# Kernel optimization log

Measured on AMD Instinct MI355X. Metric: run time of the kernel, lower is better.

Reference implementation:

```python
import jax, jax.numpy as jnp
import numpy as np

B, N, SEM, STR = 64, 512, 256, 256  # batch, tokens, sem_dim_size, str_dim_size (hidden=512)


def setup_inputs() -> dict:
    key = jax.random.key(0)
    ks = jax.random.split(key, 8)
    s = 0.02  # small init so exp(f_ij)/exp(f_i) stay well-conditioned
    return {
        "input": jax.random.normal(ks[0], (B, N, SEM + STR), jnp.float32),
        "Wp": (jax.random.normal(ks[1], (STR, STR), jnp.float32) * s),
        "bp": jnp.zeros((STR,), jnp.float32),
        "Wbil": (jax.random.normal(ks[2], (STR, STR), jnp.float32) * s),
        "bbil": jnp.zeros((), jnp.float32),
        "Wfi": (jax.random.normal(ks[3], (1, STR), jnp.float32) * s),
        "bfi": jnp.zeros((1,), jnp.float32),
        "exparam": jax.random.normal(ks[4], (1, 1, SEM), jnp.float32),
        "Wfz": (jax.random.normal(ks[5], (SEM, 2 * SEM), jnp.float32) * s),
        "bfz": jnp.zeros((SEM,), jnp.float32),
    }


def reference(input, Wp, bp, Wbil, bbil, Wfi, bfi, exparam, Wfz, bfz):
    b, n, _ = input.shape
    sem_v = input[:, :, :SEM]          # [B,N,SEM]
    str_v = input[:, :, SEM:]          # [B,N,STR]

    # NOTE: source uses tp_linear for BOTH tp and tc, and expands both with
    # unsqueeze(2), so f_ij[b,i,j] = bilinear(tp[b,i], tp[b,i]) is constant in j.
    tp = str_v @ Wp.T + bp             # [B,N,STR]
    s = jnp.einsum('bid,de,bie->bi', tp, Wbil, tp) + bbil   # [B,N]
    f_ij = jnp.broadcast_to(s[:, :, None], (b, n, n))        # [B,N,N]

    f_i = jnp.exp(str_v @ Wfi.T + bfi)[..., 0]               # [B,N]

    off = 1.0 - jnp.eye(n, dtype=input.dtype)
    A = jnp.exp(f_ij) * off                                  # zero diagonal
    deg = jnp.sum(A, axis=2)                                 # [B,N]
    L = -A + deg[:, :, None] * jnp.eye(n, dtype=input.dtype) # Laplacian
    L = L.at[:, 0, :].set(f_i)                               # root-augmented L_bar

    LLinv = jnp.linalg.inv(L)                                # [B,N,N]
    d0 = f_i * LLinv[:, :, 0]                                # root marginals [B,N]
    dg = jnp.diagonal(LLinv, axis1=-2, axis2=-1)             # [B,N]

    # tmp1 and tmp2 in the source both reduce to A[b,i,j] * diag[b,j]
    tmp = A * dg[:, None, :]
    mask1 = jnp.concatenate([jnp.zeros((n, 1)), jnp.ones((n, n - 1))], 1).astype(input.dtype)
    mask2 = jnp.concatenate([jnp.zeros((1, n)), jnp.ones((n - 1, n))], 0).astype(input.dtype)
    dx = (mask1 - mask2) * tmp                               # [B,N,N]

    d = jnp.concatenate([d0[:, None, :], dx], axis=1)        # [B,N+1,N]
    df = jnp.swapaxes(d, 1, 2)                               # [B,N,N+1]
    ssr = jnp.concatenate([jnp.broadcast_to(exparam, (b, 1, SEM)), sem_v], 1)  # [B,N+1,SEM]
    pinp = jnp.einsum('bnm,bmd->bnd', df, ssr)               # [B,N,SEM]
    # cinp = dx @ sem_v is computed in the source but never used -> omitted

    finp = jnp.concatenate([sem_v, pinp], axis=-1)           # [B,N,2*SEM]
    return jax.nn.relu(finp @ Wfz.T + bfz)                   # [B,N,SEM]
```

## Files before the change

kernel.cpp:

```cpp
#include <hip/hip_runtime.h>
#include <math.h>

#define B_    64
#define N_    512
#define SEM_  256
#define STR_  256
#define DIM_  512
#define ROWS_ (B_*N_)

#define OFF_T      0
#define OFF_QT16   65536
#define OFF_W116   98304
#define OFF_W2T    131072
#define OFF_V1     196608
#define OFF_C1     196864
#define OFF_H      197120
#define OFF_C0     197376
#define OFF_EV     197440
#define OFF_FV     230208
#define OFF_SUMP   262976
#define OFF_V2B    394048
#define OFF_ROW0   410432

typedef __bf16 bf16x8 __attribute__((ext_vector_type(8)));
typedef float  f32x4  __attribute__((ext_vector_type(4)));

__device__ __forceinline__ ushort f2b(float x) {
    return __builtin_bit_cast(ushort, (__bf16)x);
}
__device__ __forceinline__ float bflo(unsigned u) {
    return __builtin_bit_cast(float, u << 16);
}
__device__ __forceinline__ float bfhi(unsigned u) {
    return __builtin_bit_cast(float, u & 0xffff0000u);
}

__global__ __launch_bounds__(256) void k0a(
    const float* __restrict__ Wp, const float* __restrict__ bp,
    const float* __restrict__ Wbil, const float* __restrict__ Wfz,
    const float* __restrict__ exparam,
    float* __restrict__ T, ushort* __restrict__ W116, float* __restrict__ W2t,
    float* __restrict__ v1, float* __restrict__ h, float* __restrict__ c0)
{
    int t = threadIdx.x, a = blockIdx.x;
    float acc = 0.f;
    const float* wb = Wbil + a*256;
    for (int c = 0; c < 256; ++c) acc += wb[c] * Wp[c*256 + t];
    T[a*256 + t] = acc;
    W116[a*256 + t] = f2b(Wfz[a*512 + t]);
    W2t[t*256 + a] = Wfz[a*512 + 256 + t];
    if (a == 0) {
        float s = 0.f;
        const float* w2 = Wfz + t*512 + 256;
        for (int dd = 0; dd < 256; ++dd) s += w2[dd] * exparam[dd];
        v1[t] = s;
    }
    if (a == 1) {
        float g = 0.f, g2 = 0.f;
        for (int c = 0; c < 256; ++c) {
            g  += Wbil[t*256 + c] * bp[c];
            g2 += Wbil[c*256 + t] * bp[c];
        }
        h[t] = g + g2;
        __shared__ float red[256];
        red[t] = bp[t] * g;
        __syncthreads();
        for (int s2 = 128; s2 > 0; s2 >>= 1) {
            if (t < s2) red[t] += red[t + s2];
            __syncthreads();
        }
        if (t == 0) c0[0] = red[0];
    }
}

__global__ __launch_bounds__(256) void k0b(
    const float* __restrict__ Wp, const float* __restrict__ T,
    const float* __restrict__ h,
    ushort* __restrict__ Qt16, float* __restrict__ c1)
{
    int t = threadIdx.x, d = blockIdx.x;
    float acc = 0.f;
    for (int a2 = 0; a2 < 256; ++a2) acc += Wp[a2*256 + d] * T[a2*256 + t];
    Qt16[t*256 + d] = f2b(acc);
    __shared__ float red[256];
    red[t] = Wp[t*256 + d] * h[t];
    __syncthreads();
    for (int s2 = 128; s2 > 0; s2 >>= 1) {
        if (t < s2) red[t] += red[t + s2];
        __syncthreads();
    }
    if (t == 0) c1[d] = red[0];
}

__global__ __launch_bounds__(256, 3) void k_rowstats(
    const float* __restrict__ input, const ushort* __restrict__ Qt16,
    const float* __restrict__ c1, const float* __restrict__ c0,
    const float* __restrict__ Wfi, const float* __restrict__ bbil,
    const float* __restrict__ bfi, const float* __restrict__ W2t,
    float* __restrict__ Ev, float* __restrict__ fv, float* __restrict__ v2b)
{
    __shared__ __align__(16) char smem[52288];
    ushort* Ash   = (ushort*)smem;
    ushort* Ush   = (ushort*)(smem + 32768);
    float*  sdiag = (float*)(smem + 49152);
    float*  fdiag = (float*)(smem + 50176);
    float*  s0sh  = (float*)(smem + 51200);
    float*  shE0  = (float*)(smem + 52224);

    int t = threadIdx.x;
    int lane = t & 63, w = t >> 6;
    int g = lane >> 4, li = lane & 15;
    long rowbase = (long)blockIdx.x * 64;
    int b = (int)(rowbase >> 9);
    int i0 = (int)(rowbase & 511);
    const float* Ab = input + rowbase*DIM_ + SEM_;

#pragma unroll
    for (int q = 0; q < 16; ++q) {
        int v = t + 256*q;
        int r = v >> 6, c4 = v & 63;
        float4 a4 = *(const float4*)(Ab + (long)r*DIM_ + c4*4);
        ushort4 b4 = make_ushort4(f2b(a4.x), f2b(a4.y), f2b(a4.z), f2b(a4.w));
        *(ushort4*)&Ash[r*256 + ((c4*4) ^ ((r & 7) << 3))] = b4;
    }
    __syncthreads();

    f32x4 acc[4][4];
#pragma unroll
    for (int m = 0; m < 4; ++m)
#pragma unroll
        for (int n = 0; n < 4; ++n) acc[m][n] = (f32x4){0.f, 0.f, 0.f, 0.f};

    int xs = (li & 7) << 3;
#pragma unroll 2
    for (int k0 = 0; k0 < 256; k0 += 32) {
        bf16x8 af[4], bfr[4];
#pragma unroll
        for (int n = 0; n < 4; ++n)
            bfr[n] = *(const bf16x8*)&Qt16[(w*64 + n*16 + li)*256 + k0 + g*8];
#pragma unroll
        for (int m = 0; m < 4; ++m)
            af[m] = *(const bf16x8*)&Ash[(m*16 + li)*256 + ((k0 + g*8) ^ xs)];
#pragma unroll
        for (int m = 0; m < 4; ++m)
#pragma unroll
            for (int n = 0; n < 4; ++n)
                acc[m][n] = __builtin_amdgcn_mfma_f32_16x16x32_bf16(af[m], bfr[n], acc[m][n], 0, 0, 0);
    }

    float c1v[4];
#pragma unroll
    for (int n = 0; n < 4; ++n) c1v[n] = c1[w*64 + n*16 + li];

    f32x4 dacc[4], facc[4];
#pragma unroll
    for (int m = 0; m < 4; ++m) { dacc[m] = (f32x4){0.f,0.f,0.f,0.f}; facc[m] = (f32x4){0.f,0.f,0.f,0.f}; }

#pragma unroll
    for (int h = 0; h < 2; ++h) {
        if ((w >> 1) == h) {
            int cl0 = (w & 1)*64;
#pragma unroll
            for (int m = 0; m < 4; ++m)
#pragma unroll
                for (int n = 0; n < 4; ++n)
#pragma unroll
                    for (int reg = 0; reg < 4; ++reg) {
                        int row = m*16 + g*4 + reg;
                        int cl = cl0 + n*16 + li;
                        Ush[row*128 + (cl ^ ((row & 7) << 3))] = f2b(acc[m][n][reg] + c1v[n]);
                    }
        }
        __syncthreads();
        int kb = w*32 + g*8;
        int kg = h*128 + kb;
        float4 wf0 = *(const float4*)(Wfi + kg);
        float4 wf1 = *(const float4*)(Wfi + kg + 4);
        bf16x8 afw = (bf16x8){(__bf16)wf0.x, (__bf16)wf0.y, (__bf16)wf0.z, (__bf16)wf0.w,
                              (__bf16)wf1.x, (__bf16)wf1.y, (__bf16)wf1.z, (__bf16)wf1.w};
#pragma unroll
        for (int m = 0; m < 4; ++m) {
            bf16x8 afu = *(const bf16x8*)&Ush[(m*16 + li)*128 + (kb ^ xs)];
            bf16x8 bfs = *(const bf16x8*)&Ash[(m*16 + li)*256 + (kg ^ xs)];
            dacc[m] = __builtin_amdgcn_mfma_f32_16x16x32_bf16(afu, bfs, dacc[m], 0, 0, 0);
            facc[m] = __builtin_amdgcn_mfma_f32_16x16x32_bf16(afw, bfs, facc[m], 0, 0, 0);
        }
        __syncthreads();
    }

    if (g == (li >> 2)) {
        int dr = li & 3;
#pragma unroll
        for (int m = 0; m < 4; ++m) {
            float dv = dr == 0 ? dacc[m][0] : dr == 1 ? dacc[m][1] : dr == 2 ? dacc[m][2] : dacc[m][3];
            sdiag[(m*16 + li)*4 + w] = dv;
        }
    }
    if (g == 0) {
#pragma unroll
        for (int m = 0; m < 4; ++m) fdiag[(m*16 + li)*4 + w] = facc[m][0];
    }
    __syncthreads();
    if (t < 64) {
        float ss = sdiag[t*4] + sdiag[t*4+1] + sdiag[t*4+2] + sdiag[t*4+3];
        float ff = fdiag[t*4] + fdiag[t*4+1] + fdiag[t*4+2] + fdiag[t*4+3];
        float ev = expf(ss + c0[0] + bbil[0]);
        Ev[rowbase + t] = ev;
        fv[rowbase + t] = expf(ff + bfi[0]);
        if (t == 0) shE0[0] = ev;
    }

    if (i0 == 0) {
        if (t < 64)
            *(float4*)&s0sh[t*4] = *(const float4*)(input + (long)b*512*DIM_ + t*4);
        __syncthreads();
        float a2 = 0.f;
        for (int d = 0; d < 256; ++d) a2 += W2t[d*256 + t] * s0sh[d];
        v2b[b*256 + t] = shE0[0] * a2;
    }
}

__global__ __launch_bounds__(256, 3) void k_final(
    const float* __restrict__ input, const ushort* __restrict__ W116,
    const float* __restrict__ v1, const float* __restrict__ v2b,
    const float* __restrict__ Ev, const float* __restrict__ fv,
    const float* __restrict__ bfz,
    float* __restrict__ sump, float* __restrict__ row0pre,
    float* __restrict__ out)
{
    __shared__ __align__(16) char smem[41792];
    ushort* Ash    = (ushort*)smem;
    float*  Csh    = (float*)smem;
    float*  sumred = (float*)(smem + 32768);
    float*  cAs    = (float*)(smem + 40960);
    float*  cBs    = (float*)(smem + 41216);
    float*  EvL    = (float*)(smem + 41472);
    float*  wred   = (float*)(smem + 41728);

    int t = threadIdx.x;
    int lane = t & 63, w = t >> 6;
    int g = lane >> 4, li = lane & 15;
    long rowbase = (long)blockIdx.x * 64;
    int b = (int)(rowbase >> 9);
    int i0 = (int)(rowbase & 511);
    const float* Ab = input + rowbase*DIM_;

    float fsum = fv[b*512 + t] + fv[b*512 + 256 + t];
#pragma unroll
    for (int off = 32; off >= 1; off >>= 1) fsum += __shfl_down(fsum, off);
    if (lane == 0) wred[w] = fsum;
    __syncthreads();
    float invF = 1.0f / (wred[0] + wred[1] + wred[2] + wred[3]);

    if (t < 64) {
        int row = (int)rowbase + t;
        float fr = fv[row];
        float ev = Ev[row];
        EvL[t] = (i0 == 0 && t == 0) ? 0.f : ev;
        cAs[t] = fr * invF;
        cBs[t] = ((i0 + t) == 0) ? -invF
               : (1.0f + (fv[b*512] - fr)*invF) / (512.0f * ev);
    }

#pragma unroll
    for (int q = 0; q < 16; ++q) {
        int v = t + 256*q;
        int r = v >> 6, c4 = v & 63;
        float4 a4 = *(const float4*)(Ab + (long)r*DIM_ + c4*4);
        ushort4 b4 = make_ushort4(f2b(a4.x), f2b(a4.y), f2b(a4.z), f2b(a4.w));
        *(ushort4*)&Ash[r*256 + ((c4*4) ^ ((r & 7) << 3))] = b4;
    }
    __syncthreads();

    f32x4 acc[4][4];
#pragma unroll
    for (int m = 0; m < 4; ++m)
#pragma unroll
        for (int n = 0; n < 4; ++n) acc[m][n] = (f32x4){0.f, 0.f, 0.f, 0.f};

    int xs = (li & 7) << 3;
#pragma unroll 2
    for (int k0 = 0; k0 < 256; k0 += 32) {
        bf16x8 af[4], bfr[4];
#pragma unroll
        for (int n = 0; n < 4; ++n)
            bfr[n] = *(const bf16x8*)&W116[(w*64 + n*16 + li)*256 + k0 + g*8];
#pragma unroll
        for (int m = 0; m < 4; ++m)
            af[m] = *(const bf16x8*)&Ash[(m*16 + li)*256 + ((k0 + g*8) ^ xs)];
#pragma unroll
        for (int m = 0; m < 4; ++m)
#pragma unroll
            for (int n = 0; n < 4; ++n)
                acc[m][n] = __builtin_amdgcn_mfma_f32_16x16x32_bf16(af[m], bfr[n], acc[m][n], 0, 0, 0);
    }

    {
        int qq = t >> 5, c8 = t & 31;
        float p[8];
#pragma unroll
        for (int i = 0; i < 8; ++i) p[i] = 0.f;
#pragma unroll
        for (int rr = 0; rr < 8; ++rr) {
            int r = qq*8 + rr;
            float ev = EvL[r];
            uint4 uv = *(const uint4*)&Ash[r*256 + ((c8*8) ^ (rr << 3))];
            p[0] += ev * bflo(uv.x); p[1] += ev * bfhi(uv.x);
            p[2] += ev * bflo(uv.y); p[3] += ev * bfhi(uv.y);
            p[4] += ev * bflo(uv.z); p[5] += ev * bfhi(uv.z);
            p[6] += ev * bflo(uv.w); p[7] += ev * bfhi(uv.w);
        }
        *(float4*)&sumred[qq*256 + c8*8]     = (float4){p[0], p[1], p[2], p[3]};
        *(float4*)&sumred[qq*256 + c8*8 + 4] = (float4){p[4], p[5], p[6], p[7]};
    }
    __syncthreads();
    {
        float sp = 0.f;
#pragma unroll
        for (int qq = 0; qq < 8; ++qq) sp += sumred[qq*256 + t];
        sump[(long)blockIdx.x*256 + t] = sp;
    }

    float v1v[4], v2v[4], bzv[4];
#pragma unroll
    for (int n = 0; n < 4; ++n) {
        int col = w*64 + n*16 + li;
        v1v[n] = v1[col];
        v2v[n] = v2b[b*256 + col];
        bzv[n] = bfz[col];
    }

#pragma unroll
    for (int hh = 0; hh < 2; ++hh) {
        __syncthreads();
#pragma unroll
        for (int mm = 0; mm < 2; ++mm) {
            int m = hh*2 + mm;
#pragma unroll
            for (int reg = 0; reg < 4; ++reg) {
                int row = m*16 + g*4 + reg;
                int row_l = row - hh*32;
                int sw = ((row_l >> 2) & 3) << 3;
                float ca = cAs[row], cb = cBs[row];
                int irow = i0 + row;
#pragma unroll
                for (int n = 0; n < 4; ++n) {
                    int col = w*64 + n*16 + li;
                    float sel = (irow == 0) ? 0.f : v2v[n];
                    float val = acc[m][n][reg] + ca*v1v[n] + cb*sel + bzv[n];
                    if (irow == 0) row0pre[b*256 + col] = val;
                    Csh[row_l*256 + (col ^ sw)] = fmaxf(val, 0.f);
                }
            }
        }
        __syncthreads();
#pragma unroll
        for (int q = 0; q < 8; ++q) {
            int v = t + 256*q;
            int r = v >> 6, c4 = v & 63;
            int sw = ((r >> 2) & 3) << 3;
            *(float4*)(out + (rowbase + hh*32 + r)*256 + c4*4) =
                *(const float4*)&Csh[r*256 + ((c4*4) ^ sw)];
        }
    }
}

__global__ __launch_bounds__(256) void k_fix(
    const float* __restrict__ sump, const float* __restrict__ fv,
    const float* __restrict__ W2t, const float* __restrict__ row0pre,
    float* __restrict__ out)
{
    int b = blockIdx.x, t = threadIdx.x;
    __shared__ float svsh[256];
    __shared__ float redF[256];
    float a = 0.f;
#pragma unroll
    for (int p = 0; p < 8; ++p) a += sump[(long)(b*8 + p)*256 + t];
    svsh[t] = a;
    redF[t] = fv[b*512 + t] + fv[b*512 + 256 + t];
    __syncthreads();
    for (int s2 = 128; s2 > 0; s2 >>= 1) {
        if (t < s2) redF[t] += redF[t + s2];
        __syncthreads();
    }
    float invF = 1.0f / redF[0];
    float a0 = 0.f;
    for (int d = 0; d < 256; ++d) a0 += W2t[d*256 + t] * svsh[d];
    out[((long)b*512)*256 + t] = fmaxf(row0pre[b*256 + t] - invF*a0, 0.f);
}

extern "C" void kernel_launch(void* const* d_in, const int* in_sizes, int n_in,
                              void* d_out, int out_size, void* d_ws, size_t ws_size,
                              hipStream_t stream) {
    const float* input   = (const float*)d_in[0];
    const float* Wp      = (const float*)d_in[1];
    const float* bp      = (const float*)d_in[2];
    const float* Wbil    = (const float*)d_in[3];
    const float* bbil    = (const float*)d_in[4];
    const float* Wfi     = (const float*)d_in[5];
    const float* bfi     = (const float*)d_in[6];
    const float* exparam = (const float*)d_in[7];
    const float* Wfz     = (const float*)d_in[8];
    const float* bfz     = (const float*)d_in[9];
    float* ws  = (float*)d_ws;
    float* out = (float*)d_out;

    float*  T     = ws + OFF_T;
    ushort* Qt16  = (ushort*)(ws + OFF_QT16);
    ushort* W116  = (ushort*)(ws + OFF_W116);
    float*  W2t   = ws + OFF_W2T;
    float*  v1    = ws + OFF_V1;
    float*  c1    = ws + OFF_C1;
    float*  h     = ws + OFF_H;
    float*  c0    = ws + OFF_C0;
    float*  Ev    = ws + OFF_EV;
    float*  fv    = ws + OFF_FV;
    float*  sump  = ws + OFF_SUMP;
    float*  v2b   = ws + OFF_V2B;
    float*  row0p = ws + OFF_ROW0;

    k0a<<<256, 256, 0, stream>>>(Wp, bp, Wbil, Wfz, exparam, T, W116, W2t, v1, h, c0);
    k0b<<<256, 256, 0, stream>>>(Wp, T, h, Qt16, c1);
    k_rowstats<<<ROWS_/64, 256, 0, stream>>>(input, Qt16, c1, c0, Wfi, bbil, bfi, W2t, Ev, fv, v2b);
    k_final<<<ROWS_/64, 256, 0, stream>>>(input, W116, v1, v2b, Ev, fv, bfz, sump, row0p, out);
    k_fix<<<B_, 256, 0, stream>>>(sump, fv, W2t, row0p, out);
}
```

Baseline: 93.50 us.

## Fuse rowstats, final GEMM and row-0 fix into one kernel with per-batch spin barrier

Merges the row-statistics kernel, the final projection kernel and the per-batch row-0 fixup into a single kernel. The eight blocks of a batch exchange partial sums (F totals, sem sums, v2 partials) through global memory and an atomic counter with a spin-wait. This removes two launches and the Ev/fv/row0pre round trips. It relies on all 8 blocks of a batch being co-resident, which risks deadlock or stalls if scheduling does not guarantee that. It also transposes k0b's access pattern for coalescing and adds unroll pragmas.

```diff
diff --git a/kernel.cpp b/kernel.cpp
--- a/kernel.cpp
+++ b/kernel.cpp
@@ -16,11 +16,12 @@
 #define OFF_C1     196864
 #define OFF_H      197120
 #define OFF_C0     197376
-#define OFF_EV     197440
-#define OFF_FV     230208
-#define OFF_SUMP   262976
-#define OFF_V2B    394048
-#define OFF_ROW0   410432
+#define OFF_EV0    197440
+#define OFF_FV0    197504
+#define OFF_FPART  197568
+#define OFF_CNT    198080
+#define OFF_V2BR   198144
+#define OFF_SUMP   214528
 
 typedef __bf16 bf16x8 __attribute__((ext_vector_type(8)));
 typedef float  f32x4  __attribute__((ext_vector_type(4)));
@@ -40,11 +41,13 @@
     const float* __restrict__ Wbil, const float* __restrict__ Wfz,
     const float* __restrict__ exparam,
     float* __restrict__ T, ushort* __restrict__ W116, float* __restrict__ W2t,
-    float* __restrict__ v1, float* __restrict__ h, float* __restrict__ c0)
+    float* __restrict__ v1, float* __restrict__ h, float* __restrict__ c0,
+    unsigned* __restrict__ cnt)
 {
     int t = threadIdx.x, a = blockIdx.x;
     float acc = 0.f;
     const float* wb = Wbil + a*256;
+#pragma unroll 16
     for (int c = 0; c < 256; ++c) acc += wb[c] * Wp[c*256 + t];
     T[a*256 + t] = acc;
     W116[a*256 + t] = f2b(Wfz[a*512 + t]);
@@ -52,11 +55,13 @@
     if (a == 0) {
         float s = 0.f;
         const float* w2 = Wfz + t*512 + 256;
+#pragma unroll 16
         for (int dd = 0; dd < 256; ++dd) s += w2[dd] * exparam[dd];
         v1[t] = s;
     }
     if (a == 1) {
         float g = 0.f, g2 = 0.f;
+#pragma unroll 8
         for (int c = 0; c < 256; ++c) {
             g  += Wbil[t*256 + c] * bp[c];
             g2 += Wbil[c*256 + t] * bp[c];
@@ -71,6 +76,7 @@
         }
         if (t == 0) c0[0] = red[0];
     }
+    if (a == 2 && t < 64) cnt[t] = 0u;
 }
 
 __global__ __launch_bounds__(256) void k0b(
@@ -78,48 +84,60 @@
     const float* __restrict__ h,
     ushort* __restrict__ Qt16, float* __restrict__ c1)
 {
-    int t = threadIdx.x, d = blockIdx.x;
+    int t = threadIdx.x, e = blockIdx.x;
     float acc = 0.f;
-    for (int a2 = 0; a2 < 256; ++a2) acc += Wp[a2*256 + d] * T[a2*256 + t];
-    Qt16[t*256 + d] = f2b(acc);
+#pragma unroll 16
+    for (int a2 = 0; a2 < 256; ++a2) acc += Wp[a2*256 + t] * T[a2*256 + e];
+    Qt16[e*256 + t] = f2b(acc);
     __shared__ float red[256];
-    red[t] = Wp[t*256 + d] * h[t];
+    red[t] = Wp[t*256 + e] * h[t];
     __syncthreads();
     for (int s2 = 128; s2 > 0; s2 >>= 1) {
         if (t < s2) red[t] += red[t + s2];
         __syncthreads();
     }
-    if (t == 0) c1[d] = red[0];
-}
-
-__global__ __launch_bounds__(256, 3) void k_rowstats(
+    if (t == 0) c1[e] = red[0];
+}
+
+__global__ __launch_bounds__(256, 3) void k_fused(
     const float* __restrict__ input, const ushort* __restrict__ Qt16,
+    const ushort* __restrict__ W116, const float* __restrict__ W2t,
     const float* __restrict__ c1, const float* __restrict__ c0,
     const float* __restrict__ Wfi, const float* __restrict__ bbil,
-    const float* __restrict__ bfi, const float* __restrict__ W2t,
-    float* __restrict__ Ev, float* __restrict__ fv, float* __restrict__ v2b)
+    const float* __restrict__ bfi, const float* __restrict__ v1,
+    const float* __restrict__ bfz,
+    float* __restrict__ Ev0g, float* __restrict__ Fv0g,
+    float* __restrict__ Fpart, unsigned* __restrict__ cnt,
+    float* __restrict__ v2braw, float* __restrict__ sumpart,
+    float* __restrict__ out)
 {
-    __shared__ __align__(16) char smem[52288];
-    ushort* Ash   = (ushort*)smem;
-    ushort* Ush   = (ushort*)(smem + 32768);
-    float*  sdiag = (float*)(smem + 49152);
-    float*  fdiag = (float*)(smem + 50176);
-    float*  s0sh  = (float*)(smem + 51200);
-    float*  shE0  = (float*)(smem + 52224);
+    __shared__ __align__(16) char smem[53248];
+    ushort* Ash  = (ushort*)smem;
+    ushort* Ush  = (ushort*)(smem + 32768);
+    float*  rgA  = (float*)(smem + 49152);
+    float*  rgB  = (float*)(smem + 50176);
+    float*  EvL  = (float*)(smem + 51200);
+    float*  FvL  = (float*)(smem + 51456);
+    float*  cAs  = (float*)(smem + 51712);
+    float*  cBs  = (float*)(smem + 51968);
+    float*  a0sh = (float*)(smem + 52224);
 
     int t = threadIdx.x;
     int lane = t & 63, w = t >> 6;
     int g = lane >> 4, li = lane & 15;
-    long rowbase = (long)blockIdx.x * 64;
-    int b = (int)(rowbase >> 9);
-    int i0 = (int)(rowbase & 511);
-    const float* Ab = input + rowbase*DIM_ + SEM_;
+    int bk = blockIdx.x;
+    int b = bk >> 3, rt = bk & 7;
+    long rowbase = (long)b*512 + rt*64;
+    int i0 = rt*64;
+    const float* AbS = input + rowbase*DIM_ + SEM_;
+    const float* AbM = input + rowbase*DIM_;
+    int xs = (li & 7) << 3;
 
 #pragma unroll
     for (int q = 0; q < 16; ++q) {
         int v = t + 256*q;
         int r = v >> 6, c4 = v & 63;
-        float4 a4 = *(const float4*)(Ab + (long)r*DIM_ + c4*4);
+        float4 a4 = *(const float4*)(AbS + (long)r*DIM_ + c4*4);
         ushort4 b4 = make_ushort4(f2b(a4.x), f2b(a4.y), f2b(a4.z), f2b(a4.w));
         *(ushort4*)&Ash[r*256 + ((c4*4) ^ ((r & 7) << 3))] = b4;
     }
@@ -131,8 +149,7 @@
 #pragma unroll
         for (int n = 0; n < 4; ++n) acc[m][n] = (f32x4){0.f, 0.f, 0.f, 0.f};
 
-    int xs = (li & 7) << 3;
-#pragma unroll 2
+#pragma unroll 4
     for (int k0 = 0; k0 < 256; k0 += 32) {
         bf16x8 af[4], bfr[4];
 #pragma unroll
@@ -148,154 +165,88 @@
                 acc[m][n] = __builtin_amdgcn_mfma_f32_16x16x32_bf16(af[m], bfr[n], acc[m][n], 0, 0, 0);
     }
 
-    float c1v[4];
-#pragma unroll
-    for (int n = 0; n < 4; ++n) c1v[n] = c1[w*64 + n*16 + li];
-
-    f32x4 dacc[4], facc[4];
-#pragma unroll
-    for (int m = 0; m < 4; ++m) { dacc[m] = (f32x4){0.f,0.f,0.f,0.f}; facc[m] = (f32x4){0.f,0.f,0.f,0.f}; }
-
-#pragma unroll
-    for (int h = 0; h < 2; ++h) {
-        if ((w >> 1) == h) {
-            int cl0 = (w & 1)*64;
-#pragma unroll
-            for (int m = 0; m < 4; ++m)
-#pragma unroll
-                for (int n = 0; n < 4; ++n)
-#pragma unroll
-                    for (int reg = 0; reg < 4; ++reg) {
-                        int row = m*16 + g*4 + reg;
-                        int cl = cl0 + n*16 + li;
-                        Ush[row*128 + (cl ^ ((row & 7) << 3))] = f2b(acc[m][n][reg] + c1v[n]);
-                    }
-        }
-        __syncthreads();
-        int kb = w*32 + g*8;
-        int kg = h*128 + kb;
-        float4 wf0 = *(const float4*)(Wfi + kg);
-        float4 wf1 = *(const float4*)(Wfi + kg + 4);
-        bf16x8 afw = (bf16x8){(__bf16)wf0.x, (__bf16)wf0.y, (__bf16)wf0.z, (__bf16)wf0.w,
-                              (__bf16)wf1.x, (__bf16)wf1.y, (__bf16)wf1.z, (__bf16)wf1.w};
-#pragma unroll
-        for (int m = 0; m < 4; ++m) {
-            bf16x8 afu = *(const bf16x8*)&Ush[(m*16 + li)*128 + (kb ^ xs)];
-            bf16x8 bfs = *(const bf16x8*)&Ash[(m*16 + li)*256 + (kg ^ xs)];
-            dacc[m] = __builtin_amdgcn_mfma_f32_16x16x32_bf16(afu, bfs, dacc[m], 0, 0, 0);
-            facc[m] = __builtin_amdgcn_mfma_f32_16x16x32_bf16(afw, bfs, facc[m], 0, 0, 0);
-        }
-        __syncthreads();
-    }
-
-    if (g == (li >> 2)) {
-        int dr = li & 3;
-#pragma unroll
-        for (int m = 0; m < 4; ++m) {
-            float dv = dr == 0 ? dacc[m][0] : dr == 1 ? dacc[m][1] : dr == 2 ? dacc[m][2] : dacc[m][3];
-            sdiag[(m*16 + li)*4 + w] = dv;
-        }
-    }
-    if (g == 0) {
-#pragma unroll
-        for (int m = 0; m < 4; ++m) fdiag[(m*16 + li)*4 + w] = facc[m][0];
-    }
-    __syncthreads();
+    {
+        float c1v[4];
+#pragma unroll
+        for (int n = 0; n < 4; ++n) c1v[n] = c1[w*64 + n*16 + li];
+
+        f32x4 dacc[4], facc[4];
+#pragma unroll
+        for (int m = 0; m < 4; ++m) { dacc[m] = (f32x4){0.f,0.f,0.f,0.f}; facc[m] = (f32x4){0.f,0.f,0.f,0.f}; }
+
+#pragma unroll
+        for (int hv = 0; hv < 2; ++hv) {
+            if ((w >> 1) == hv) {
+                int cl0 = (w & 1)*64;
+#pragma unroll
+                for (int m = 0; m < 4; ++m)
+#pragma unroll
+                    for (int n = 0; n < 4; ++n)
+#pragma unroll
+                        for (int reg = 0; reg < 4; ++reg) {
+                            int row = m*16 + g*4 + reg;
+                            int cl = cl0 + n*16 + li;
+                            Ush[row*128 + (cl ^ ((row & 7) << 3))] = f2b(acc[m][n][reg] + c1v[n]);
+                        }
+            }
+            __syncthreads();
+            int kb = w*32 + g*8;
+            int kg = hv*128 + kb;
+            float4 wf0 = *(const float4*)(Wfi + kg);
+            float4 wf1 = *(const float4*)(Wfi + kg + 4);
+            bf16x8 afw = (bf16x8){(__bf16)wf0.x, (__bf16)wf0.y, (__bf16)wf0.z, (__bf16)wf0.w,
+                                  (__bf16)wf1.x, (__bf16)wf1.y, (__bf16)wf1.z, (__bf16)wf1.w};
+#pragma unroll
+            for (int m = 0; m < 4; ++m) {
+                bf16x8 afu = *(const bf16x8*)&Ush[(m*16 + li)*128 + (kb ^ xs)];
+                bf16x8 bfs = *(const bf16x8*)&Ash[(m*16 + li)*256 + (kg ^ xs)];
+                dacc[m] = __builtin_amdgcn_mfma_f32_16x16x32_bf16(afu, bfs, dacc[m], 0, 0, 0);
+                facc[m] = __builtin_amdgcn_mfma_f32_16x16x32_bf16(afw, bfs, facc[m], 0, 0, 0);
+            }
+            __syncthreads();
+        }
+
+        if (g == (li >> 2)) {
+            int dr = li & 3;
+#pragma unroll
+            for (int m = 0; m < 4; ++m) {
+                float dv = dr == 0 ? dacc[m][0] : dr == 1 ? dacc[m][1] : dr == 2 ? dacc[m][2] : dacc[m][3];
+                rgA[(m*16 + li)*4 + w] = dv;
+            }
+        }
+        if (g == 0) {
+#pragma unroll
+            for (int m = 0; m < 4; ++m) rgB[(m*16 + li)*4 + w] = facc[m][0];
+        }
+    }
+    __syncthreads();
+
     if (t < 64) {
-        float ss = sdiag[t*4] + sdiag[t*4+1] + sdiag[t*4+2] + sdiag[t*4+3];
-        float ff = fdiag[t*4] + fdiag[t*4+1] + fdiag[t*4+2] + fdiag[t*4+3];
+        float ss = rgA[t*4] + rgA[t*4+1] + rgA[t*4+2] + rgA[t*4+3];
+        float ff = rgB[t*4] + rgB[t*4+1] + rgB[t*4+2] + rgB[t*4+3];
         float ev = expf(ss + c0[0] + bbil[0]);
-        Ev[rowbase + t] = ev;
-        fv[rowbase + t] = expf(ff + bfi[0]);
-        if (t == 0) shE0[0] = ev;
-    }
-
-    if (i0 == 0) {
-        if (t < 64)
-            *(float4*)&s0sh[t*4] = *(const float4*)(input + (long)b*512*DIM_ + t*4);
-        __syncthreads();
-        float a2 = 0.f;
-        for (int d = 0; d < 256; ++d) a2 += W2t[d*256 + t] * s0sh[d];
-        v2b[b*256 + t] = shE0[0] * a2;
-    }
-}
-
-__global__ __launch_bounds__(256, 3) void k_final(
-    const float* __restrict__ input, const ushort* __restrict__ W116,
-    const float* __restrict__ v1, const float* __restrict__ v2b,
-    const float* __restrict__ Ev, const float* __restrict__ fv,
-    const float* __restrict__ bfz,
-    float* __restrict__ sump, float* __restrict__ row0pre,
-    float* __restrict__ out)
-{
-    __shared__ __align__(16) char smem[41792];
-    ushort* Ash    = (ushort*)smem;
-    float*  Csh    = (float*)smem;
-    float*  sumred = (float*)(smem + 32768);
-    float*  cAs    = (float*)(smem + 40960);
-    float*  cBs    = (float*)(smem + 41216);
-    float*  EvL    = (float*)(smem + 41472);
-    float*  wred   = (float*)(smem + 41728);
-
-    int t = threadIdx.x;
-    int lane = t & 63, w = t >> 6;
-    int g = lane >> 4, li = lane & 15;
-    long rowbase = (long)blockIdx.x * 64;
-    int b = (int)(rowbase >> 9);
-    int i0 = (int)(rowbase & 511);
-    const float* Ab = input + rowbase*DIM_;
-
-    float fsum = fv[b*512 + t] + fv[b*512 + 256 + t];
-#pragma unroll
-    for (int off = 32; off >= 1; off >>= 1) fsum += __shfl_down(fsum, off);
-    if (lane == 0) wred[w] = fsum;
-    __syncthreads();
-    float invF = 1.0f / (wred[0] + wred[1] + wred[2] + wred[3]);
-
-    if (t < 64) {
-        int row = (int)rowbase + t;
-        float fr = fv[row];
-        float ev = Ev[row];
-        EvL[t] = (i0 == 0 && t == 0) ? 0.f : ev;
-        cAs[t] = fr * invF;
-        cBs[t] = ((i0 + t) == 0) ? -invF
-               : (1.0f + (fv[b*512] - fr)*invF) / (512.0f * ev);
-    }
-
+        float fr = expf(ff + bfi[0]);
+        FvL[t] = fr;
+        EvL[t] = (rt == 0 && t == 0) ? 0.f : ev;
+        if (rt == 0 && t == 0) { Ev0g[b] = ev; Fv0g[b] = fr; }
+        float fs = fr;
+#pragma unroll
+        for (int off = 32; off >= 1; off >>= 1) fs += __shfl_down(fs, off);
+        if (t == 0) Fpart[bk] = fs;
+        *(float4*)&rgA[t*4] = *(const float4*)(input + (long)b*512*DIM_ + t*4);
+    }
 #pragma unroll
     for (int q = 0; q < 16; ++q) {
         int v = t + 256*q;
         int r = v >> 6, c4 = v & 63;
-        float4 a4 = *(const float4*)(Ab + (long)r*DIM_ + c4*4);
+        float4 a4 = *(const float4*)(AbM + (long)r*DIM_ + c4*4);
         ushort4 b4 = make_ushort4(f2b(a4.x), f2b(a4.y), f2b(a4.z), f2b(a4.w));
         *(ushort4*)&Ash[r*256 + ((c4*4) ^ ((r & 7) << 3))] = b4;
     }
     __syncthreads();
 
-    f32x4 acc[4][4];
-#pragma unroll
-    for (int m = 0; m < 4; ++m)
-#pragma unroll
-        for (int n = 0; n < 4; ++n) acc[m][n] = (f32x4){0.f, 0.f, 0.f, 0.f};
-
-    int xs = (li & 7) << 3;
-#pragma unroll 2
-    for (int k0 = 0; k0 < 256; k0 += 32) {
-        bf16x8 af[4], bfr[4];
-#pragma unroll
-        for (int n = 0; n < 4; ++n)
-            bfr[n] = *(const bf16x8*)&W116[(w*64 + n*16 + li)*256 + k0 + g*8];
-#pragma unroll
-        for (int m = 0; m < 4; ++m)
-            af[m] = *(const bf16x8*)&Ash[(m*16 + li)*256 + ((k0 + g*8) ^ xs)];
-#pragma unroll
-        for (int m = 0; m < 4; ++m)
-#pragma unroll
-            for (int n = 0; n < 4; ++n)
-                acc[m][n] = __builtin_amdgcn_mfma_f32_16x16x32_bf16(af[m], bfr[n], acc[m][n], 0, 0, 0);
-    }
-
     {
+        float* sumred = (float*)Ush;
         int qq = t >> 5, c8 = t & 31;
         float p[8];
 #pragma unroll
@@ -312,13 +263,84 @@
         }
         *(float4*)&sumred[qq*256 + c8*8]     = (float4){p[0], p[1], p[2], p[3]};
         *(float4*)&sumred[qq*256 + c8*8 + 4] = (float4){p[4], p[5], p[6], p[7]};
-    }
-    __syncthreads();
+
+        int colL = t & 31, part = t >> 5;
+        float vp = 0.f;
+#pragma unroll 8
+        for (int dd = 0; dd < 32; ++dd) {
+            int d = part*32 + dd;
+            vp += W2t[d*256 + rt*32 + colL] * rgA[d];
+        }
+        rgB[colL*8 + part] = vp;
+    }
+    __syncthreads();
+
     {
+        float* sumred = (float*)Ush;
         float sp = 0.f;
 #pragma unroll
         for (int qq = 0; qq < 8; ++qq) sp += sumred[qq*256 + t];
-        sump[(long)blockIdx.x*256 + t] = sp;
+        sumpart[(long)bk*256 + t] = sp;
+        if (t < 32) {
+            float v = 0.f;
+#pragma unroll
+            for (int p = 0; p < 8; ++p) v += rgB[t*8 + p];
+            v2braw[b*256 + rt*32 + t] = v;
+        }
+    }
+    __threadfence();
+    __syncthreads();
+    if (t == 0)
+        __hip_atomic_fetch_add(&cnt[b], 1u, __ATOMIC_RELEASE, __HIP_MEMORY_SCOPE_AGENT);
+
+    while (__hip_atomic_load(&cnt[b], __ATOMIC_ACQUIRE, __HIP_MEMORY_SCOPE_AGENT) < 8u)
+        __builtin_amdgcn_s_sleep(2);
+
+    float Ftot = 0.f;
+#pragma unroll
+    for (int p = 0; p < 8; ++p) Ftot += Fpart[b*8 + p];
+    float invF = 1.0f / Ftot;
+    float E0 = Ev0g[b], f0v = Fv0g[b];
+    if (t < 64) {
+        float fr = FvL[t], ev = EvL[t];
+        cAs[t] = fr * invF;
+        cBs[t] = ((i0 + t) == 0) ? -invF
+               : (1.0f + (f0v - fr)*invF) / (512.0f * ev);
+    }
+    if (rt == 0) {
+        float sv = 0.f;
+#pragma unroll
+        for (int p = 0; p < 8; ++p) sv += sumpart[(long)(b*8 + p)*256 + t];
+        rgA[t] = sv;
+    }
+    __syncthreads();
+
+#pragma unroll
+    for (int m = 0; m < 4; ++m)
+#pragma unroll
+        for (int n = 0; n < 4; ++n) acc[m][n] = (f32x4){0.f, 0.f, 0.f, 0.f};
+
+#pragma unroll 4
+    for (int k0 = 0; k0 < 256; k0 += 32) {
+        bf16x8 af[4], bfr[4];
+#pragma unroll
+        for (int n = 0; n < 4; ++n)
+            bfr[n] = *(const bf16x8*)&W116[(w*64 + n*16 + li)*256 + k0 + g*8];
+#pragma unroll
+        for (int m = 0; m < 4; ++m)
+            af[m] = *(const bf16x8*)&Ash[(m*16 + li)*256 + ((k0 + g*8) ^ xs)];
+#pragma unroll
+        for (int m = 0; m < 4; ++m)
+#pragma unroll
+            for (int n = 0; n < 4; ++n)
+                acc[m][n] = __builtin_amdgcn_mfma_f32_16x16x32_bf16(af[m], bfr[n], acc[m][n], 0, 0, 0);
+    }
+
+    if (rt == 0) {
+        float a0 = 0.f;
+#pragma unroll 16
+        for (int d = 0; d < 256; ++d) a0 += W2t[d*256 + t] * rgA[d];
+        a0sh[t] = a0;
     }
 
     float v1v[4], v2v[4], bzv[4];
@@ -326,10 +348,11 @@
     for (int n = 0; n < 4; ++n) {
         int col = w*64 + n*16 + li;
         v1v[n] = v1[col];
-        v2v[n] = v2b[b*256 + col];
+        v2v[n] = E0 * v2braw[b*256 + col];
         bzv[n] = bfz[col];
     }
 
+    float* Csh = (float*)Ash;
 #pragma unroll
     for (int hh = 0; hh < 2; ++hh) {
         __syncthreads();
@@ -346,9 +369,8 @@
 #pragma unroll
                 for (int n = 0; n < 4; ++n) {
                     int col = w*64 + n*16 + li;
-                    float sel = (irow == 0) ? 0.f : v2v[n];
+                    float sel = (irow == 0) ? a0sh[col] : v2v[n];
                     float val = acc[m][n][reg] + ca*v1v[n] + cb*sel + bzv[n];
-                    if (irow == 0) row0pre[b*256 + col] = val;
                     Csh[row_l*256 + (col ^ sw)] = fmaxf(val, 0.f);
                 }
             }
@@ -363,30 +385,6 @@
                 *(const float4*)&Csh[r*256 + ((c4*4) ^ sw)];
         }
     }
-}
-
-__global__ __launch_bounds__(256) void k_fix(
-    const float* __restrict__ sump, const float* __restrict__ fv,
-    const float* __restrict__ W2t, const float* __restrict__ row0pre,
-    float* __restrict__ out)
-{
-    int b = blockIdx.x, t = threadIdx.x;
-    __shared__ float svsh[256];
-    __shared__ float redF[256];
-    float a = 0.f;
-#pragma unroll
-    for (int p = 0; p < 8; ++p) a += sump[(long)(b*8 + p)*256 + t];
-    svsh[t] = a;
-    redF[t] = fv[b*512 + t] + fv[b*512 + 256 + t];
-    __syncthreads();
-    for (int s2 = 128; s2 > 0; s2 >>= 1) {
-        if (t < s2) redF[t] += redF[t + s2];
-        __syncthreads();
-    }
-    float invF = 1.0f / redF[0];
-    float a0 = 0.f;
-    for (int d = 0; d < 256; ++d) a0 += W2t[d*256 + t] * svsh[d];
-    out[((long)b*512)*256 + t] = fmaxf(row0pre[b*256 + t] - invF*a0, 0.f);
 }
 
 extern "C" void kernel_launch(void* const* d_in, const int* in_sizes, int n_in,
@@ -405,23 +403,23 @@
     float* ws  = (float*)d_ws;
     float* out = (float*)d_out;
 
-    float*  T     = ws + OFF_T;
-    ushort* Qt16  = (ushort*)(ws + OFF_QT16);
-    ushort* W116  = (ushort*)(ws + OFF_W116);
-    float*  W2t   = ws + OFF_W2T;
-    float*  v1    = ws + OFF_V1;
-    float*  c1    = ws + OFF_C1;
-    float*  h     = ws + OFF_H;
-    float*  c0    = ws + OFF_C0;
-    float*  Ev    = ws + OFF_EV;
-    float*  fv    = ws + OFF_FV;
-    float*  sump  = ws + OFF_SUMP;
-    float*  v2b   = ws + OFF_V2B;
-    float*  row0p = ws + OFF_ROW0;
-
-    k0a<<<256, 256, 0, stream>>>(Wp, bp, Wbil, Wfz, exparam, T, W116, W2t, v1, h, c0);
+    float*    T      = ws + OFF_T;
+    ushort*   Qt16   = (ushort*)(ws + OFF_QT16);
+    ushort*   W116   = (ushort*)(ws + OFF_W116);
+    float*    W2t    = ws + OFF_W2T;
+    float*    v1     = ws + OFF_V1;
+    float*    c1     = ws + OFF_C1;
+    float*    h      = ws + OFF_H;
+    float*    c0     = ws + OFF_C0;
+    float*    Ev0g   = ws + OFF_EV0;
+    float*    Fv0g   = ws + OFF_FV0;
+    float*    Fpart  = ws + OFF_FPART;
+    unsigned* cnt    = (unsigned*)(ws + OFF_CNT);
+    float*    v2braw = ws + OFF_V2BR;
+    float*    sumpart= ws + OFF_SUMP;
+
+    k0a<<<256, 256, 0, stream>>>(Wp, bp, Wbil, Wfz, exparam, T, W116, W2t, v1, h, c0, cnt);
     k0b<<<256, 256, 0, stream>>>(Wp, T, h, Qt16, c1);
-    k_rowstats<<<ROWS_/64, 256, 0, stream>>>(input, Qt16, c1, c0, Wfi, bbil, bfi, W2t, Ev, fv, v2b);
-    k_final<<<ROWS_/64, 256, 0, stream>>>(input, W116, v1, v2b, Ev, fv, bfz, sump, row0p, out);
-    k_fix<<<B_, 256, 0, stream>>>(sump, fv, W2t, row0p, out);
-}
+    k_fused<<<ROWS_/64, 256, 0, stream>>>(input, Qt16, W116, W2t, c1, c0, Wfi, bbil, bfi,
+                                          v1, bfz, Ev0g, Fv0g, Fpart, cnt, v2braw, sumpart, out);
+}
```

Result: slower. 183.6 us (+96.4%).

## Stage weight tiles through padded LDS and coalesce prep-kernel accesses

Applied to the files above, without the earlier changes.

The GEMM B operand (Qt16/W116) is now copied per k-step into a padded shared-memory tile and read from LDS, replacing per-lane strided global loads. In k_final the A-tile load and GEMM move ahead of the row-coefficient setup. k0b is re-indexed so each thread reads consecutive Wp elements and writes contiguous Qt16 rows, and several scalar loops get unroll pragmas. The cost is two extra barriers per k-step and more shared memory per block, which may reduce occupancy.

```diff
diff --git a/kernel.cpp b/kernel.cpp
--- a/kernel.cpp
+++ b/kernel.cpp
@@ -45,6 +45,7 @@
     int t = threadIdx.x, a = blockIdx.x;
     float acc = 0.f;
     const float* wb = Wbil + a*256;
+#pragma unroll 16
     for (int c = 0; c < 256; ++c) acc += wb[c] * Wp[c*256 + t];
     T[a*256 + t] = acc;
     W116[a*256 + t] = f2b(Wfz[a*512 + t]);
@@ -52,11 +53,13 @@
     if (a == 0) {
         float s = 0.f;
         const float* w2 = Wfz + t*512 + 256;
+#pragma unroll 16
         for (int dd = 0; dd < 256; ++dd) s += w2[dd] * exparam[dd];
         v1[t] = s;
     }
     if (a == 1) {
         float g = 0.f, g2 = 0.f;
+#pragma unroll 8
         for (int c = 0; c < 256; ++c) {
             g  += Wbil[t*256 + c] * bp[c];
             g2 += Wbil[c*256 + t] * bp[c];
@@ -78,18 +81,19 @@
     const float* __restrict__ h,
     ushort* __restrict__ Qt16, float* __restrict__ c1)
 {
-    int t = threadIdx.x, d = blockIdx.x;
+    int t = threadIdx.x, e = blockIdx.x;
     float acc = 0.f;
-    for (int a2 = 0; a2 < 256; ++a2) acc += Wp[a2*256 + d] * T[a2*256 + t];
-    Qt16[t*256 + d] = f2b(acc);
+#pragma unroll 16
+    for (int a2 = 0; a2 < 256; ++a2) acc += Wp[a2*256 + t] * T[a2*256 + e];
+    Qt16[e*256 + t] = f2b(acc);
     __shared__ float red[256];
-    red[t] = Wp[t*256 + d] * h[t];
+    red[t] = Wp[t*256 + e] * h[t];
     __syncthreads();
     for (int s2 = 128; s2 > 0; s2 >>= 1) {
         if (t < s2) red[t] += red[t + s2];
         __syncthreads();
     }
-    if (t == 0) c1[d] = red[0];
+    if (t == 0) c1[e] = red[0];
 }
 
 __global__ __launch_bounds__(256, 3) void k_rowstats(
@@ -99,8 +103,9 @@
     const float* __restrict__ bfi, const float* __restrict__ W2t,
     float* __restrict__ Ev, float* __restrict__ fv, float* __restrict__ v2b)
 {
-    __shared__ __align__(16) char smem[52288];
+    __shared__ __align__(16) char smem[53248];
     ushort* Ash   = (ushort*)smem;
+    ushort* Bsm   = (ushort*)(smem + 32768);
     ushort* Ush   = (ushort*)(smem + 32768);
     float*  sdiag = (float*)(smem + 49152);
     float*  fdiag = (float*)(smem + 50176);
@@ -114,6 +119,7 @@
     int b = (int)(rowbase >> 9);
     int i0 = (int)(rowbase & 511);
     const float* Ab = input + rowbase*DIM_ + SEM_;
+    int xs = (li & 7) << 3;
 
 #pragma unroll
     for (int q = 0; q < 16; ++q) {
@@ -123,7 +129,6 @@
         ushort4 b4 = make_ushort4(f2b(a4.x), f2b(a4.y), f2b(a4.z), f2b(a4.w));
         *(ushort4*)&Ash[r*256 + ((c4*4) ^ ((r & 7) << 3))] = b4;
     }
-    __syncthreads();
 
     f32x4 acc[4][4];
 #pragma unroll
@@ -131,21 +136,27 @@
 #pragma unroll
         for (int n = 0; n < 4; ++n) acc[m][n] = (f32x4){0.f, 0.f, 0.f, 0.f};
 
-    int xs = (li & 7) << 3;
-#pragma unroll 2
     for (int k0 = 0; k0 < 256; k0 += 32) {
+#pragma unroll
+        for (int q = 0; q < 4; ++q) {
+            int v = t + 256*q;
+            int n = v >> 2, c = v & 3;
+            *(uint4*)&Bsm[n*40 + c*8] = *(const uint4*)&Qt16[n*256 + k0 + c*8];
+        }
+        __syncthreads();
         bf16x8 af[4], bfr[4];
-#pragma unroll
-        for (int n = 0; n < 4; ++n)
-            bfr[n] = *(const bf16x8*)&Qt16[(w*64 + n*16 + li)*256 + k0 + g*8];
 #pragma unroll
         for (int m = 0; m < 4; ++m)
             af[m] = *(const bf16x8*)&Ash[(m*16 + li)*256 + ((k0 + g*8) ^ xs)];
 #pragma unroll
+        for (int n = 0; n < 4; ++n)
+            bfr[n] = *(const bf16x8*)&Bsm[(w*64 + n*16 + li)*40 + g*8];
+#pragma unroll
         for (int m = 0; m < 4; ++m)
 #pragma unroll
             for (int n = 0; n < 4; ++n)
                 acc[m][n] = __builtin_amdgcn_mfma_f32_16x16x32_bf16(af[m], bfr[n], acc[m][n], 0, 0, 0);
+        __syncthreads();
     }
 
     float c1v[4];
@@ -157,8 +168,8 @@
     for (int m = 0; m < 4; ++m) { dacc[m] = (f32x4){0.f,0.f,0.f,0.f}; facc[m] = (f32x4){0.f,0.f,0.f,0.f}; }
 
 #pragma unroll
-    for (int h = 0; h < 2; ++h) {
-        if ((w >> 1) == h) {
+    for (int hv = 0; hv < 2; ++hv) {
+        if ((w >> 1) == hv) {
             int cl0 = (w & 1)*64;
 #pragma unroll
             for (int m = 0; m < 4; ++m)
@@ -173,7 +184,7 @@
         }
         __syncthreads();
         int kb = w*32 + g*8;
-        int kg = h*128 + kb;
+        int kg = hv*128 + kb;
         float4 wf0 = *(const float4*)(Wfi + kg);
         float4 wf1 = *(const float4*)(Wfi + kg + 4);
         bf16x8 afw = (bf16x8){(__bf16)wf0.x, (__bf16)wf0.y, (__bf16)wf0.z, (__bf16)wf0.w,
@@ -215,6 +226,7 @@
             *(float4*)&s0sh[t*4] = *(const float4*)(input + (long)b*512*DIM_ + t*4);
         __syncthreads();
         float a2 = 0.f;
+#pragma unroll 8
         for (int d = 0; d < 256; ++d) a2 += W2t[d*256 + t] * s0sh[d];
         v2b[b*256 + t] = shE0[0] * a2;
     }
@@ -228,9 +240,10 @@
     float* __restrict__ sump, float* __restrict__ row0pre,
     float* __restrict__ out)
 {
-    __shared__ __align__(16) char smem[41792];
+    __shared__ __align__(16) char smem[53248];
     ushort* Ash    = (ushort*)smem;
     float*  Csh    = (float*)smem;
+    ushort* Bsm    = (ushort*)(smem + 32768);
     float*  sumred = (float*)(smem + 32768);
     float*  cAs    = (float*)(smem + 40960);
     float*  cBs    = (float*)(smem + 41216);
@@ -244,6 +257,45 @@
     int b = (int)(rowbase >> 9);
     int i0 = (int)(rowbase & 511);
     const float* Ab = input + rowbase*DIM_;
+    int xs = (li & 7) << 3;
+
+#pragma unroll
+    for (int q = 0; q < 16; ++q) {
+        int v = t + 256*q;
+        int r = v >> 6, c4 = v & 63;
+        float4 a4 = *(const float4*)(Ab + (long)r*DIM_ + c4*4);
+        ushort4 b4 = make_ushort4(f2b(a4.x), f2b(a4.y), f2b(a4.z), f2b(a4.w));
+        *(ushort4*)&Ash[r*256 + ((c4*4) ^ ((r & 7) << 3))] = b4;
+    }
+
+    f32x4 acc[4][4];
+#pragma unroll
+    for (int m = 0; m < 4; ++m)
+#pragma unroll
+        for (int n = 0; n < 4; ++n) acc[m][n] = (f32x4){0.f, 0.f, 0.f, 0.f};
+
+    for (int k0 = 0; k0 < 256; k0 += 32) {
+#pragma unroll
+        for (int q = 0; q < 4; ++q) {
+            int v = t + 256*q;
+            int n = v >> 2, c = v & 3;
+            *(uint4*)&Bsm[n*40 + c*8] = *(const uint4*)&W116[n*256 + k0 + c*8];
+        }
+        __syncthreads();
+        bf16x8 af[4], bfr[4];
+#pragma unroll
+        for (int m = 0; m < 4; ++m)
+            af[m] = *(const bf16x8*)&Ash[(m*16 + li)*256 + ((k0 + g*8) ^ xs)];
+#pragma unroll
+        for (int n = 0; n < 4; ++n)
+            bfr[n] = *(const bf16x8*)&Bsm[(w*64 + n*16 + li)*40 + g*8];
+#pragma unroll
+        for (int m = 0; m < 4; ++m)
+#pragma unroll
+            for (int n = 0; n < 4; ++n)
+                acc[m][n] = __builtin_amdgcn_mfma_f32_16x16x32_bf16(af[m], bfr[n], acc[m][n], 0, 0, 0);
+        __syncthreads();
+    }
 
     float fsum = fv[b*512 + t] + fv[b*512 + 256 + t];
 #pragma unroll
@@ -261,39 +313,7 @@
         cBs[t] = ((i0 + t) == 0) ? -invF
                : (1.0f + (fv[b*512] - fr)*invF) / (512.0f * ev);
     }
-
-#pragma unroll
-    for (int q = 0; q < 16; ++q) {
-        int v = t + 256*q;
-        int r = v >> 6, c4 = v & 63;
-        float4 a4 = *(const float4*)(Ab + (long)r*DIM_ + c4*4);
-        ushort4 b4 = make_ushort4(f2b(a4.x), f2b(a4.y), f2b(a4.z), f2b(a4.w));
-        *(ushort4*)&Ash[r*256 + ((c4*4) ^ ((r & 7) << 3))] = b4;
-    }
-    __syncthreads();
-
-    f32x4 acc[4][4];
-#pragma unroll
-    for (int m = 0; m < 4; ++m)
-#pragma unroll
-        for (int n = 0; n < 4; ++n) acc[m][n] = (f32x4){0.f, 0.f, 0.f, 0.f};
-
-    int xs = (li & 7) << 3;
-#pragma unroll 2
-    for (int k0 = 0; k0 < 256; k0 += 32) {
-        bf16x8 af[4], bfr[4];
-#pragma unroll
-        for (int n = 0; n < 4; ++n)
-            bfr[n] = *(const bf16x8*)&W116[(w*64 + n*16 + li)*256 + k0 + g*8];
-#pragma unroll
-        for (int m = 0; m < 4; ++m)
-            af[m] = *(const bf16x8*)&Ash[(m*16 + li)*256 + ((k0 + g*8) ^ xs)];
-#pragma unroll
-        for (int m = 0; m < 4; ++m)
-#pragma unroll
-            for (int n = 0; n < 4; ++n)
-                acc[m][n] = __builtin_amdgcn_mfma_f32_16x16x32_bf16(af[m], bfr[n], acc[m][n], 0, 0, 0);
-    }
+    __syncthreads();
 
     {
         int qq = t >> 5, c8 = t & 31;
@@ -385,6 +405,7 @@
     }
     float invF = 1.0f / redF[0];
     float a0 = 0.f;
+#pragma unroll 8
     for (int d = 0; d < 256; ++d) a0 += W2t[d*256 + t] * svsh[d];
     out[((long)b*512)*256 + t] = fmaxf(row0pre[b*256 + t] - invF*a0, 0.f);
 }
```

New measurement: 97.93 us. 4.7% more time.
